# Kernel optimization log

Measured on AMD Instinct MI355X. Metric: run time of the kernel, lower is better.

## Reference

```python
import jax, jax.numpy as jnp
import numpy as np

NUM_HEADS = 12
SS_ATTN_ITER = 1
EPS = 1e-12  # F.normalize default eps


def _l2norm(x):
    n = jnp.linalg.norm(x, axis=-1, keepdims=True)
    return x / jnp.maximum(n, EPS)


def setup_inputs() -> dict:
    key = jax.random.key(0)
    k1, k2, k3, k4 = jax.random.split(key, 4)
    N, B, C = 1569, 8, 768
    x = jax.random.normal(k1, (N, B, C), dtype=jnp.float32)
    Wqkv = jax.random.normal(k2, (3 * C, C), dtype=jnp.float32) * 0.02
    Wproj = jax.random.normal(k3, (C, C), dtype=jnp.float32) * 0.02
    bproj = jax.random.normal(k4, (C,), dtype=jnp.float32) * 0.02
    return {"x": x, "Wqkv": Wqkv, "Wproj": Wproj, "bproj": bproj}


def _forward(x, Wqkv, Wproj, bproj):
    # x: [N, B, C] -> [B, N, C] (module does x.transpose(0, 1))
    xb = jnp.swapaxes(x, 0, 1)
    B, N, C = xb.shape
    H = NUM_HEADS
    hd = C // H
    scale = hd ** (-0.5)

    # qkv projection (no bias), split into per-head q, k, v: [B, H, N, hd]
    qkv = (xb @ Wqkv.T).reshape(B, N, 3, H, hd)
    qkv = jnp.transpose(qkv, (2, 0, 3, 1, 4))
    q, k, v = qkv[0], qkv[1], qkv[2]

    # ---- original attention branch ----
    attn_ori = jax.nn.softmax(jnp.einsum('bhnd,bhmd->bhnm', q, k) * scale, axis=-1)
    x_ori = jnp.einsum('bhnm,bhmd->bhnd', attn_ori, v)
    x_ori = jnp.transpose(x_ori, (0, 2, 1, 3)).reshape(B, N, C)
    x_ori = x_ori @ Wproj.T + bproj

    # ---- self-self attention branches ----
    # inv_temp = mean over tokens of ||x||_2, per batch: [B, 1, 1, 1]
    pre_norm = jnp.mean(jnp.linalg.norm(xb, axis=-1), axis=-1)
    inv_temp = pre_norm[:, None, None, None] * scale

    def branch(xs):
        for _ in range(SS_ATTN_ITER):
            xs = _l2norm(xs)
            a = jax.nn.softmax(jnp.einsum('bhnd,bhmd->bhnm', xs, xs) * inv_temp, axis=-1)
            xs = jnp.einsum('bhnm,bhmd->bhnd', a, xs)
        xs = _l2norm(xs)
        a = jax.nn.softmax(jnp.einsum('bhnd,bhmd->bhnm', xs, xs) * inv_temp, axis=-1)
        return jnp.einsum('bhnm,bhmd->bhnd', a, v)

    xs = (branch(v) + branch(k) + branch(q)) / 3.0
    x_out = jnp.transpose(xs, (0, 2, 1, 3)).reshape(B, N, C)
    x_out = x_out @ Wproj.T + bproj

    # return in original [N, B, C] layout
    return jnp.swapaxes(x_out, 0, 1), jnp.swapaxes(x_ori, 0, 1)


def reference(x, Wqkv, Wproj, bproj):
    return _forward(x, Wqkv, Wproj, bproj)
```

## Files before the change

kernel.cpp:

```cpp
#include <hip/hip_runtime.h>
#include <stdint.h>

#define NTOK 1569
#define BB 8
#define CC 768
#define HH 12
#define HD 64
#define NBH (BB*HH)
#define NROW (NTOK*BB)
#define NCHUNK 25
#define NVEC (NBH*NTOK)
#define LASTV 33

typedef unsigned short ushort_t;
static const size_t SZ = (size_t)NROW * CC;

using f32x4 = __attribute__((ext_vector_type(4))) float;
using i32x4 = __attribute__((ext_vector_type(4))) int;
using i32x2 = __attribute__((ext_vector_type(2))) int;
using hfrag = __attribute__((ext_vector_type(8))) _Float16;

__device__ __forceinline__ float exp2_fast(float x){
  float r;
  asm("v_exp_f32 %0, %1" : "=v"(r) : "v"(x));
  return r;
}

__global__ __launch_bounds__(256) void prenorm_kernel(const float* __restrict__ x,
                                                      float* __restrict__ pre)
{
  const int b = blockIdx.y;
  const int wave = threadIdx.x >> 6, lane = threadIdx.x & 63;
  const int g = blockIdx.x * 4 + wave;
  float local = 0.f;
  for (int n = g; n < NTOK; n += 200){
    const float* xp = x + ((size_t)n * BB + b) * CC + lane * 4;
    float ss = 0.f;
    #pragma unroll
    for (int e = 0; e < 3; e++){
      f32x4 vv = *(const f32x4*)(xp + 256*e);
      ss += vv[0]*vv[0] + vv[1]*vv[1] + vv[2]*vv[2] + vv[3]*vv[3];
    }
    #pragma unroll
    for (int off = 1; off < 64; off <<= 1) ss += __shfl_xor(ss, off);
    local += sqrtf(ss);
  }
  if (lane == 0) atomicAdd(&pre[b], local);
}

__global__ __launch_bounds__(256) void cvt_f16(const float* __restrict__ in,
                                               ushort_t* __restrict__ out,
                                               int n8, float scl)
{
  const int i = blockIdx.x * 256 + threadIdx.x;
  if (i >= n8) return;
  const float* p = in + (size_t)i * 8;
  f32x4 a = *(const f32x4*)p, b = *(const f32x4*)(p + 4);
  union { _Float16 h[8]; i32x4 v; } u;
  #pragma unroll
  for (int e = 0; e < 4; e++){
    u.h[e]   = (_Float16)(a[e] * scl);
    u.h[4+e] = (_Float16)(b[e] * scl);
  }
  *(i32x4*)(out + (size_t)i * 8) = u.v;
}

__global__ __launch_bounds__(256) void gemm768(
    const ushort_t* __restrict__ A, const ushort_t* __restrict__ Bm,
    ushort_t* __restrict__ q, ushort_t* __restrict__ k, ushort_t* __restrict__ v,
    float* __restrict__ outp, const float* __restrict__ bias, int mode)
{
  __shared__ __align__(16) ushort_t As[8192];
  __shared__ __align__(16) ushort_t Bs[8192];

  const int jtN = gridDim.y;
  const int lin = blockIdx.y * 99 + blockIdx.x;
  const int T  = 99 * jtN;
  const int qq = T >> 3, rr = T & 7;
  const int c  = lin & 7, ii = lin >> 3;
  const int start = c*qq + (c < rr ? c : rr);
  const int idx = start + ii;
  const int mt = idx / jtN, jt = idx - mt*jtN;

  const int tid = threadIdx.x;
  const int w = tid >> 6, lane = tid & 63;
  const int l16 = lane & 15, lq = lane >> 4;

  const int srow = tid & 127, shalf = tid >> 7;
  int ga = mt*128 + srow; if (ga > NROW-1) ga = NROW-1;
  const ushort_t* ap = A  + (size_t)ga * CC + shalf*32;
  const ushort_t* bp = Bm + (size_t)(jt*128 + srow) * CC + shalf*32;
  const int rb = srow >> 4, r16 = srow & 15;

  const int wr = (w >> 1) * 4, wc = (w & 1) * 4;

  f32x4 acc[4][4] = {};
  for (int kt = 0; kt < 12; kt++){
    #pragma unroll
    for (int i = 0; i < 4; i++){
      const int kq = shalf*4 + i;
      *(i32x4*)&As[((rb*8 + kq)*16 + r16)*8] = *(const i32x4*)(ap + kt*64 + i*8);
      *(i32x4*)&Bs[((rb*8 + kq)*16 + r16)*8] = *(const i32x4*)(bp + kt*64 + i*8);
    }
    __syncthreads();
    #pragma unroll
    for (int ks = 0; ks < 2; ks++){
      hfrag af[4], bf[4];
      #pragma unroll
      for (int rt = 0; rt < 4; rt++)
        af[rt] = *(const hfrag*)&As[(((wr+rt)*8 + ks*4 + lq)*16 + l16)*8];
      #pragma unroll
      for (int ct = 0; ct < 4; ct++)
        bf[ct] = *(const hfrag*)&Bs[(((wc+ct)*8 + ks*4 + lq)*16 + l16)*8];
      #pragma unroll
      for (int rt = 0; rt < 4; rt++)
        #pragma unroll
        for (int ct = 0; ct < 4; ct++)
          acc[rt][ct] = __builtin_amdgcn_mfma_f32_16x16x32_f16(af[rt], bf[ct], acc[rt][ct], 0, 0, 0);
    }
    __syncthreads();
  }

  const int mbase = mt*128 + (w >> 1)*64;
  const int jbase = jt*128 + (w & 1)*64;
  #pragma unroll
  for (int ct = 0; ct < 4; ct++){
    const int j = jbase + ct*16 + l16;
    if (mode == 0){
      const int s = j / 768, jj = j - s*768;
      const int h = jj >> 6, d = jj & 63;
      ushort_t* op = (s == 0) ? q : (s == 1) ? k : v;
      #pragma unroll
      for (int rt = 0; rt < 4; rt++)
        #pragma unroll
        for (int r = 0; r < 4; r++){
          const int m = mbase + rt*16 + lq*4 + r;
          if (m < NROW){
            const int n = m >> 3, b = m & 7;
            union { _Float16 h16; ushort_t u; } cv;
            cv.h16 = (_Float16)acc[rt][ct][r];
            op[((size_t)(b*HH + h) * NTOK + n) * HD + d] = cv.u;
          }
        }
    } else {
      const float bv = bias[j];
      #pragma unroll
      for (int rt = 0; rt < 4; rt++)
        #pragma unroll
        for (int r = 0; r < 4; r++){
          const int m = mbase + rt*16 + lq*4 + r;
          if (m < NROW) outp[(size_t)m * CC + j] = acc[rt][ct][r] + bv;
        }
    }
  }
}

__global__ __launch_bounds__(256) void l2norm_kernel(const ushort_t* __restrict__ in,
                                                     ushort_t* __restrict__ out,
                                                     int mode)
{
  const int vec = blockIdx.x * 8 + (threadIdx.x >> 5);
  const int lane = threadIdx.x & 31;
  if (vec >= NVEC) return;
  size_t iaddr;
  if (mode == 0){
    iaddr = (size_t)vec * HD + lane*2;
  } else {
    const int b = vec / (HH*NTOK);
    const int rem = vec - b*(HH*NTOK);
    const int h = rem / NTOK, n = rem - h*NTOK;
    iaddr = (size_t)(n*BB + b) * CC + h*HD + lane*2;
  }
  union { ushort_t u[2]; uint32_t pk; _Float16 h[2]; } uv;
  uv.pk = *(const uint32_t*)(in + iaddr);
  const float a = (float)uv.h[0], c = (float)uv.h[1];
  float ss = a*a + c*c;
  #pragma unroll
  for (int off = 1; off < 32; off <<= 1) ss += __shfl_xor(ss, off);
  const float inv = 1.0f / fmaxf(sqrtf(ss), 1e-12f);
  union { _Float16 h[2]; uint32_t pk; } ov;
  ov.h[0] = (_Float16)(a * inv);
  ov.h[1] = (_Float16)(c * inv);
  *(uint32_t*)(out + (size_t)vec * HD + lane*2) = ov.pk;
}

__global__ __launch_bounds__(256) void attn_mfma(
    const ushort_t* __restrict__ X, const ushort_t* __restrict__ Y,
    const ushort_t* __restrict__ Z, void* __restrict__ outp,
    const float* __restrict__ pre, float tf, int mode, int accum)
{
  __shared__ __align__(16) ushort_t Ks[64*64];
  __shared__ __align__(16) ushort_t Vt[64*64];
  __shared__ __align__(16) ushort_t Pt[128*64];

  const int lin  = blockIdx.y * 13 + blockIdx.x;
  const int nl   = (lin & 7) * 156 + (lin >> 3);
  const int bh   = nl / 13;
  const int qblk = nl - bh * 13;

  const int b = bh / HH, h = bh - (bh / HH) * HH;
  const float temp = (pre ? pre[b] * tf : tf) * 1.4426950408889634f;
  const size_t base = (size_t)bh * NTOK * HD;
  const int row0 = qblk * 128;
  const int tid = threadIdx.x;
  const int w = tid >> 6, lane = tid & 63;
  const int l16 = lane & 15, lq = lane >> 4;
  const int xk = (l16 & 7) << 4;

  hfrag qf[2][2];
  #pragma unroll
  for (int qt = 0; qt < 2; qt++){
    int r = row0 + w*32 + qt*16 + l16; if (r > NTOK-1) r = NTOK-1;
    const ushort_t* qp = X + base + (size_t)r*HD + lq*8;
    qf[qt][0] = *(const hfrag*)qp;
    qf[qt][1] = *(const hfrag*)(qp + 32);
  }

  const int skey = tid & 63, sseg = tid >> 6;
  const int kx = (skey & 7) << 4;
  const int vd2 = (tid & 31) * 2;
  const int vko = (tid >> 5) * 8;

  i32x4 kr0, kr1;
  uint32_t L[8];

  auto LOADR = [&](int ch){
    int kg = ch*64 + skey; if (kg > NTOK-1) kg = NTOK-1;
    const ushort_t* kp = Y + base + (size_t)kg*HD + sseg*16;
    kr0 = *(const i32x4*)kp;
    kr1 = *(const i32x4*)(kp + 8);
    #pragma unroll
    for (int j = 0; j < 8; j++){
      int vg = ch*64 + vko + j; if (vg > NTOK-1) vg = NTOK-1;
      L[j] = *(const uint32_t*)(Z + base + (size_t)vg*HD + vd2);
    }
  };
  auto STORER = [&](){
    char* kbp = (char*)Ks + skey*128;
    *(i32x4*)(kbp + ((sseg*32     ) ^ kx)) = kr0;
    *(i32x4*)(kbp + ((sseg*32 + 16) ^ kx)) = kr1;
    i32x4 vlo, vhi;
    #pragma unroll
    for (int cc = 0; cc < 4; cc++){
      const uint32_t Aw = L[2*cc], Bw = L[2*cc+1];
      vlo[cc] = (int)((Aw & 0xffffu) | (Bw << 16));
      vhi[cc] = (int)((Aw >> 16) | (Bw & 0xffff0000u));
    }
    char* vbp = (char*)Vt;
    *(i32x4*)(vbp + vd2*128     + ((vko*2) ^ ((vd2 & 7) << 4)))     = vlo;
    *(i32x4*)(vbp + (vd2+1)*128 + ((vko*2) ^ (((vd2+1) & 7) << 4))) = vhi;
  };

  f32x4 acc[2][4] = {};
  float lsum[2] = {0.f, 0.f};

  LOADR(0);
  STORER();
  __syncthreads();

  for (int ch = 0; ch < NCHUNK; ch++){
    if (ch + 1 < NCHUNK) LOADR(ch + 1);

    const bool lastch = (ch == NCHUNK-1);
    #pragma unroll
    for (int kt4 = 0; kt4 < 4; kt4++){
      f32x4 s0 = {}, s1 = {};
      #pragma unroll
      for (int ks = 0; ks < 2; ks++){
        hfrag kf = *(const hfrag*)((const char*)Ks + (kt4*16 + l16)*128
                                   + ((ks*64 + lq*16) ^ xk));
        s0 = __builtin_amdgcn_mfma_f32_16x16x32_f16(kf, qf[0][ks], s0, 0, 0, 0);
        s1 = __builtin_amdgcn_mfma_f32_16x16x32_f16(kf, qf[1][ks], s1, 0, 0, 0);
      }
      const int kb = kt4*16 + lq*4;
      #pragma unroll
      for (int qt = 0; qt < 2; qt++){
        const f32x4 sv = qt ? s1 : s0;
        float p0 = exp2_fast(sv[0] * temp);
        float p1 = exp2_fast(sv[1] * temp);
        float p2 = exp2_fast(sv[2] * temp);
        float p3 = exp2_fast(sv[3] * temp);
        if (lastch){
          if (kb + 0 >= LASTV) p0 = 0.f;
          if (kb + 1 >= LASTV) p1 = 0.f;
          if (kb + 2 >= LASTV) p2 = 0.f;
          if (kb + 3 >= LASTV) p3 = 0.f;
        }
        lsum[qt] += p0 + p1 + p2 + p3;
        union { _Float16 hh[4]; i32x2 v2; } pw;
        pw.hh[0] = (_Float16)p0; pw.hh[1] = (_Float16)p1;
        pw.hh[2] = (_Float16)p2; pw.hh[3] = (_Float16)p3;
        *(i32x2*)((char*)Pt + (w*32 + qt*16 + l16)*128
                  + ((kt4*32 + lq*8) ^ xk)) = pw.v2;
      }
    }

    #pragma unroll
    for (int ks = 0; ks < 2; ks++){
      const int cb = (ks*64 + lq*16) ^ xk;
      hfrag pa0 = *(const hfrag*)((const char*)Pt + (w*32 +      l16)*128 + cb);
      hfrag pa1 = *(const hfrag*)((const char*)Pt + (w*32 + 16 + l16)*128 + cb);
      #pragma unroll
      for (int dt4 = 0; dt4 < 4; dt4++){
        hfrag vf = *(const hfrag*)((const char*)Vt + (dt4*16 + l16)*128 + cb);
        acc[0][dt4] = __builtin_amdgcn_mfma_f32_16x16x32_f16(pa0, vf, acc[0][dt4], 0, 0, 0);
        acc[1][dt4] = __builtin_amdgcn_mfma_f32_16x16x32_f16(pa1, vf, acc[1][dt4], 0, 0, 0);
      }
    }
    __syncthreads();
    if (ch + 1 < NCHUNK){
      STORER();
      __syncthreads();
    }
  }

  float lfin[2];
  #pragma unroll
  for (int qt = 0; qt < 2; qt++){
    float lt = lsum[qt];
    lt += __shfl_xor(lt, 16);
    lt += __shfl_xor(lt, 32);
    lfin[qt] = lt;
  }

  #pragma unroll
  for (int qt = 0; qt < 2; qt++)
    #pragma unroll
    for (int r = 0; r < 4; r++){
      const float lv = __int_as_float(
          __builtin_amdgcn_ds_bpermute((lq*4 + r) * 4, __float_as_int(lfin[qt])));
      const int n = row0 + w*32 + qt*16 + lq*4 + r;
      if (n < NTOK){
        const float inv = 1.0f / lv;
        const size_t rbase = (size_t)(n*BB + b) * CC + h*HD;
        if (mode == 0){
          ushort_t* yo = (ushort_t*)outp;
          #pragma unroll
          for (int dt4 = 0; dt4 < 4; dt4++){
            union { _Float16 h16; ushort_t u; } cv;
            cv.h16 = (_Float16)(acc[qt][dt4][r] * inv);
            yo[rbase + dt4*16 + l16] = cv.u;
          }
        } else {
          float* ao = (float*)outp;
          #pragma unroll
          for (int dt4 = 0; dt4 < 4; dt4++){
            float o = acc[qt][dt4][r] * inv;
            if (accum) o += ao[rbase + dt4*16 + l16];
            ao[rbase + dt4*16 + l16] = o;
          }
        }
      }
    }
}

extern "C" void kernel_launch(void* const* d_in, const int* in_sizes, int n_in,
                              void* d_out, int out_size, void* d_ws, size_t ws_size,
                              hipStream_t stream)
{
  (void)in_sizes; (void)n_in; (void)out_size; (void)ws_size;

  const float* x     = (const float*)d_in[0];
  const float* wqkv  = (const float*)d_in[1];
  const float* wproj = (const float*)d_in[2];
  const float* bias  = (const float*)d_in[3];
  float* out = (float*)d_out;

  ushort_t* x16  = (ushort_t*)d_ws;
  ushort_t* wq16 = x16 + SZ;
  ushort_t* wp16 = wq16 + (size_t)2304*768;
  ushort_t* qb   = wp16 + (size_t)768*768;
  ushort_t* kb   = qb + SZ;
  ushort_t* vb   = kb + SZ;
  ushort_t* xh   = vb + SZ;
  ushort_t* y16  = xh + SZ;
  float*    acc  = (float*)(y16 + SZ);
  float*    pre  = acc + SZ;

  hipMemsetAsync(pre, 0, BB * sizeof(float), stream);

  cvt_f16<<<(int)(SZ/8 + 255)/256, 256, 0, stream>>>(x, x16, (int)(SZ/8), 1.0f);
  cvt_f16<<<(2304*768/8 + 255)/256, 256, 0, stream>>>(wqkv, wq16, 2304*768/8, 1.0f);
  cvt_f16<<<(768*768/8 + 255)/256, 256, 0, stream>>>(wproj, wp16, 768*768/8, 1.0f);
  prenorm_kernel<<<dim3(50, 8), 256, 0, stream>>>(x, pre);

  gemm768<<<dim3(99, 18), 256, 0, stream>>>(x16, wq16, qb, kb, vb, nullptr, nullptr, 0);

  const float SCALE = 0.125f;
  const float FACT  = SCALE / (float)NTOK;
  const dim3 AG(13, 96);

  attn_mfma<<<AG, 256, 0, stream>>>(qb, kb, vb, y16, nullptr, SCALE, 0, 0);
  gemm768<<<dim3(99, 6), 256, 0, stream>>>(y16, wp16, nullptr, nullptr, nullptr,
      out + (size_t)NTOK * BB * CC, bias, 1);

  const ushort_t* srcs[3] = { qb, kb, vb };
  for (int sI = 0; sI < 3; sI++){
    l2norm_kernel<<<NVEC/8, 256, 0, stream>>>(srcs[sI], xh, 0);
    attn_mfma<<<AG, 256, 0, stream>>>(xh, xh, xh, y16, pre, FACT, 0, 0);
    l2norm_kernel<<<NVEC/8, 256, 0, stream>>>(y16, xh, 1);
    attn_mfma<<<AG, 256, 0, stream>>>(xh, xh, vb, acc, pre, FACT, 1, sI == 0 ? 0 : 1);
  }

  cvt_f16<<<(int)(SZ/8 + 255)/256, 256, 0, stream>>>(acc, y16, (int)(SZ/8), 1.0f/3.0f);
  gemm768<<<dim3(99, 6), 256, 0, stream>>>(y16, wp16, nullptr, nullptr, nullptr,
      out, bias, 1);
}
```

Baseline: 1.192 ms.

## Double-buffer K/V tiles in LDS and compute softmax row sums via MFMA

Adds a second shared-memory buffer for the K and V tiles so the next chunk can be stored while the current one is being consumed, dropping one barrier per chunk. The softmax denominator is now taken from an extra MFMA of the fp16 probability tile against a ones vector, replacing the scalar running sum and the final shuffle/bpermute reduction. The cost is more LDS, which may lower occupancy. The denominator is now summed from the fp16-rounded probabilities rather than the fp32 values, which shifts numerics slightly. Pt is still a single buffer written each chunk with no barrier before the rewrite, so there is a possible race between waves.

```diff
diff --git a/kernel.cpp b/kernel.cpp
--- a/kernel.cpp
+++ b/kernel.cpp
@@ -189,8 +189,8 @@
     const ushort_t* __restrict__ Z, void* __restrict__ outp,
     const float* __restrict__ pre, float tf, int mode, int accum)
 {
-  __shared__ __align__(16) ushort_t Ks[64*64];
-  __shared__ __align__(16) ushort_t Vt[64*64];
+  __shared__ __align__(16) ushort_t Ks[2][64*64];
+  __shared__ __align__(16) ushort_t Vt[2][64*64];
   __shared__ __align__(16) ushort_t Pt[128*64];
 
   const int lin  = blockIdx.y * 13 + blockIdx.x;
@@ -216,6 +216,10 @@
     qf[qt][1] = *(const hfrag*)(qp + 32);
   }
 
+  hfrag ones;
+  #pragma unroll
+  for (int e = 0; e < 8; e++) ones[e] = (_Float16)1.0f;
+
   const int skey = tid & 63, sseg = tid >> 6;
   const int kx = (skey & 7) << 4;
   const int vd2 = (tid & 31) * 2;
@@ -235,8 +239,8 @@
       L[j] = *(const uint32_t*)(Z + base + (size_t)vg*HD + vd2);
     }
   };
-  auto STORER = [&](){
-    char* kbp = (char*)Ks + skey*128;
+  auto STORER = [&](int bf){
+    char* kbp = (char*)Ks[bf] + skey*128;
     *(i32x4*)(kbp + ((sseg*32     ) ^ kx)) = kr0;
     *(i32x4*)(kbp + ((sseg*32 + 16) ^ kx)) = kr1;
     i32x4 vlo, vhi;
@@ -246,19 +250,22 @@
       vlo[cc] = (int)((Aw & 0xffffu) | (Bw << 16));
       vhi[cc] = (int)((Aw >> 16) | (Bw & 0xffff0000u));
     }
-    char* vbp = (char*)Vt;
+    char* vbp = (char*)Vt[bf];
     *(i32x4*)(vbp + vd2*128     + ((vko*2) ^ ((vd2 & 7) << 4)))     = vlo;
     *(i32x4*)(vbp + (vd2+1)*128 + ((vko*2) ^ (((vd2+1) & 7) << 4))) = vhi;
   };
 
   f32x4 acc[2][4] = {};
-  float lsum[2] = {0.f, 0.f};
+  f32x4 acc1[2] = {};
 
   LOADR(0);
-  STORER();
+  STORER(0);
   __syncthreads();
 
   for (int ch = 0; ch < NCHUNK; ch++){
+    const int cur = ch & 1;
+    const char* Kc = (const char*)Ks[cur];
+    const char* Vc = (const char*)Vt[cur];
     if (ch + 1 < NCHUNK) LOADR(ch + 1);
 
     const bool lastch = (ch == NCHUNK-1);
@@ -267,7 +274,7 @@
       f32x4 s0 = {}, s1 = {};
       #pragma unroll
       for (int ks = 0; ks < 2; ks++){
-        hfrag kf = *(const hfrag*)((const char*)Ks + (kt4*16 + l16)*128
+        hfrag kf = *(const hfrag*)(Kc + (kt4*16 + l16)*128
                                    + ((ks*64 + lq*16) ^ xk));
         s0 = __builtin_amdgcn_mfma_f32_16x16x32_f16(kf, qf[0][ks], s0, 0, 0, 0);
         s1 = __builtin_amdgcn_mfma_f32_16x16x32_f16(kf, qf[1][ks], s1, 0, 0, 0);
@@ -286,7 +293,6 @@
           if (kb + 2 >= LASTV) p2 = 0.f;
           if (kb + 3 >= LASTV) p3 = 0.f;
         }
-        lsum[qt] += p0 + p1 + p2 + p3;
         union { _Float16 hh[4]; i32x2 v2; } pw;
         pw.hh[0] = (_Float16)p0; pw.hh[1] = (_Float16)p1;
         pw.hh[2] = (_Float16)p2; pw.hh[3] = (_Float16)p3;
@@ -302,36 +308,27 @@
       hfrag pa1 = *(const hfrag*)((const char*)Pt + (w*32 + 16 + l16)*128 + cb);
       #pragma unroll
       for (int dt4 = 0; dt4 < 4; dt4++){
-        hfrag vf = *(const hfrag*)((const char*)Vt + (dt4*16 + l16)*128 + cb);
+        hfrag vf = *(const hfrag*)(Vc + (dt4*16 + l16)*128 + cb);
         acc[0][dt4] = __builtin_amdgcn_mfma_f32_16x16x32_f16(pa0, vf, acc[0][dt4], 0, 0, 0);
         acc[1][dt4] = __builtin_amdgcn_mfma_f32_16x16x32_f16(pa1, vf, acc[1][dt4], 0, 0, 0);
       }
-    }
-    __syncthreads();
+      acc1[0] = __builtin_amdgcn_mfma_f32_16x16x32_f16(pa0, ones, acc1[0], 0, 0, 0);
+      acc1[1] = __builtin_amdgcn_mfma_f32_16x16x32_f16(pa1, ones, acc1[1], 0, 0, 0);
+    }
+
     if (ch + 1 < NCHUNK){
-      STORER();
+      STORER(cur ^ 1);
       __syncthreads();
     }
   }
 
-  float lfin[2];
-  #pragma unroll
-  for (int qt = 0; qt < 2; qt++){
-    float lt = lsum[qt];
-    lt += __shfl_xor(lt, 16);
-    lt += __shfl_xor(lt, 32);
-    lfin[qt] = lt;
-  }
-
   #pragma unroll
   for (int qt = 0; qt < 2; qt++)
     #pragma unroll
     for (int r = 0; r < 4; r++){
-      const float lv = __int_as_float(
-          __builtin_amdgcn_ds_bpermute((lq*4 + r) * 4, __float_as_int(lfin[qt])));
       const int n = row0 + w*32 + qt*16 + lq*4 + r;
       if (n < NTOK){
-        const float inv = 1.0f / lv;
+        const float inv = 1.0f / acc1[qt][r];
         const size_t rbase = (size_t)(n*BB + b) * CC + h*HD;
         if (mode == 0){
           ushort_t* yo = (ushort_t*)outp;
```

New measurement: 1.157 ms. 3.0% less time.
